# Kernel tuning notes

Hardware: AMD Instinct MI355X
Metric: run time of the kernel (lower is better)

Reference implementation:

```python
import jax, jax.numpy as jnp
import numpy as np

B, T, D = 4, 1024, 768
HW = 32            # H = W = sqrt(T)
DS = D // 16       # d_state = 48
CHUNK = 8          # items_each_chunk (must divide W)


def _ln(x, w, b, eps=1e-5):
    mu = x.mean(-1, keepdims=True)
    var = ((x - mu) ** 2).mean(-1, keepdims=True)
    return (x - mu) / jnp.sqrt(var + eps) * w + b


def _conv1x1(x, w):  # x: (B,C,H,W), w: (O,C)
    return jnp.einsum('bchw,oc->bohw', x, w)


def _dwconv(x, w, b, pad):  # depthwise conv, w: (C,1,k,k)
    y = jax.lax.conv_general_dilated(
        x, w, (1, 1), [(pad, pad), (pad, pad)],
        dimension_numbers=('NCHW', 'OIHW', 'NCHW'),
        feature_group_count=x.shape[1])
    if b is not None:
        y = y + b[None, :, None, None]
    return y


def _norm_gates(Gl, Gm, Gr):
    gl, gm, gr = jax.nn.sigmoid(Gl), jax.nn.sigmoid(Gm), jax.nn.sigmoid(Gr)
    s = gl + gm + gr
    s = s.at[:, :, 0, :].set(gm[:, :, 0, :] + gr[:, :, 0, :])    # top row: no h-1 neighbor
    s = s.at[:, :, -1, :].set(gl[:, :, -1, :] + gm[:, :, -1, :])  # bottom row: no h+1 neighbor
    s = jnp.maximum(s, 1e-7)
    return gl / s, gm / s, gr / s


def _gspn_scan(X, L, Gl, Gm, Gr, chunk):
    # GateRecurrent2dnoind: scan along W in independent chunks of `chunk` columns.
    # H[:, :, h, t] = L*X + Gl*Hprev[h-1] + Gm*Hprev[h] + Gr*Hprev[h+1], Hprev=0 at chunk start.
    b, c, h, w = X.shape
    nc = w // chunk

    def to_scan(a):  # (B,C,H,W) -> (chunk, B, C, H, nc)
        return a.reshape(b, c, h, nc, chunk).transpose(4, 0, 1, 2, 3)

    xs, ls, gls, gms, grs = map(to_scan, (X, L, Gl, Gm, Gr))

    def step(hprev, inp):
        x, l, gl, gm, gr = inp
        h_up = jnp.pad(hprev[:, :, :-1], ((0, 0), (0, 0), (1, 0), (0, 0)))
        h_dn = jnp.pad(hprev[:, :, 1:], ((0, 0), (0, 0), (0, 1), (0, 0)))
        hn = l * x + gl * h_up + gm * hprev + gr * h_dn
        return hn, hn

    _, ys = jax.lax.scan(step, jnp.zeros((b, c, h, nc), X.dtype), (xs, ls, gls, gms, grs))
    return ys.transpose(1, 2, 3, 4, 0).reshape(b, c, h, w)


def setup_inputs() -> dict:
    key = jax.random.key(0)
    ks = jax.random.split(key, 16)
    s = 0.02
    return {
        'hidden_states': jax.random.normal(ks[0], (B, T, D), jnp.float32),
        'norm_w': jnp.ones((D,), jnp.float32),
        'norm_b': jnp.zeros((D,), jnp.float32),
        'in_proj_w': jax.random.normal(ks[1], (D, D), jnp.float32) * s,
        'conv7_w': jax.random.normal(ks[2], (D, 1, 7, 7), jnp.float32) * s,
        'conv7_b': jnp.zeros((D,), jnp.float32),
        'xdown_w': jax.random.normal(ks[3], (DS, D), jnp.float32) * s,
        'wup_w': jax.random.normal(ks[4], (12 * D, DS), jnp.float32) * s,
        'lup_w': jax.random.normal(ks[5], (4 * D, DS), jnp.float32) * s,
        'uup_w': jax.random.normal(ks[6], (4 * D, DS), jnp.float32) * s,
        'dcoef_w': jax.random.normal(ks[7], (4 * D, DS), jnp.float32) * s,
        'm_w': jax.random.normal(ks[8], (4,), jnp.float32) * 0.25,
        'outconv_w': jax.random.normal(ks[9], (D, D), jnp.float32) * s,
        'outdconv_w': jax.random.normal(ks[10], (D, 1, 3, 3), jnp.float32) * s,
        'outproj_w': jax.random.normal(ks[11], (D, D), jnp.float32) * s,
    }


def reference(hidden_states, norm_w, norm_b, in_proj_w, conv7_w, conv7_b,
              xdown_w, wup_w, lup_w, uup_w, dcoef_w, m_w,
              outconv_w, outdconv_w, outproj_w):
    b, t, d = hidden_states.shape
    hh = ww = HW
    shortcut = hidden_states
    x = _ln(shortcut, norm_w, norm_b)                      # (B,T,D)
    x = x.transpose(0, 2, 1).reshape(b, d, hh, ww)         # (B,D,H,W)
    x = _conv1x1(x, in_proj_w)
    x = _dwconv(x, conv7_w, conv7_b, 3)
    xp = _conv1x1(x, xdown_w)                              # (B,ds,H,W)
    ws = _conv1x1(xp, wup_w)                               # (B,12D,H,W)
    Ls = _conv1x1(xp, lup_w)                               # (B,4D,H,W)
    Us = _conv1x1(xp, uup_w)
    Ds = _conv1x1(xp, dcoef_w)
    # 4 scan directions: [x, x^T, flip_w(x), flip_w(x^T)]
    x_hwwh = jnp.stack([x, x.transpose(0, 1, 3, 2)], axis=1)       # (B,2,D,H,W)
    xs = jnp.concatenate([x_hwwh, x_hwwh[..., ::-1]], axis=1)      # (B,4,D,H,W)
    xs = xs.reshape(b, 4 * d, hh, ww)
    Gl, Gm, Gr = ws[:, :4 * d], ws[:, 4 * d:8 * d], ws[:, 8 * d:]
    gl, gm, gr = _norm_gates(Gl, Gm, Gr)
    out = _gspn_scan(xs, Ls, gl, gm, gr, CHUNK)
    out = out * Us + xs * Ds
    out = out.reshape(b, 4, d, hh, ww)
    out = jnp.einsum('bkdhw,k->bdhw', out, m_w)            # m_conv (1x1 over 4 dirs)
    out = _conv1x1(out, outconv_w)
    out = _dwconv(out, outdconv_w, None, 1)
    out = out * jax.nn.relu(out)
    out = out.reshape(b, d, t).transpose(0, 2, 1)
    out = out @ outproj_w.T
    return out, shortcut
```

## Files before the change

### kernel.cpp

```cpp
#include <hip/hip_runtime.h>

typedef unsigned short u16;
typedef unsigned int u32;
typedef __attribute__((ext_vector_type(8))) short short8v;
typedef __attribute__((ext_vector_type(4))) float f32x4;

#define DD 768
#define PP 1024
#define NTOK 4096
#define ASN 520

__device__ __forceinline__ u16 f2bf(float f) {
  u32 u = __builtin_bit_cast(u32, f);
  u += 0x7fffu + ((u >> 16) & 1u);
  return (u16)(u >> 16);
}
__device__ __forceinline__ float b2f(u16 v) {
  return __builtin_bit_cast(float, (u32)v << 16);
}
__device__ __forceinline__ u32 pk_trunc(float fa, float fb) {
  return __builtin_amdgcn_perm(__builtin_bit_cast(u32, fa), __builtin_bit_cast(u32, fb), 0x07060302u);
}
__device__ __forceinline__ float ex8(const short8v& v, int j) {
  const u32 dw = ((const u32*)&v)[j >> 1];
  return __builtin_bit_cast(float, (j & 1) ? (dw & 0xffff0000u) : (dw << 16));
}

__global__ __launch_bounds__(256) void prep_ln_k(const float* __restrict__ hs,
                                                 const float* __restrict__ gw, const float* __restrict__ gb,
                                                 u16* __restrict__ lnout, float* __restrict__ shortcut,
                                                 const float* __restrict__ win, u16* __restrict__ wInB,
                                                 const float* __restrict__ wout, u16* __restrict__ wOutB,
                                                 const float* __restrict__ wprj, u16* __restrict__ wPrjB,
                                                 const float* __restrict__ xdw, u16* __restrict__ wXdB,
                                                 const float* __restrict__ wup, const float* __restrict__ lup,
                                                 const float* __restrict__ uup, const float* __restrict__ dco,
                                                 u16* __restrict__ wB) {
  const int id = blockIdx.x;
  const int t = threadIdx.x;
  if (id < 4096) {
    const int tok = id;
    const float* xr = hs + (size_t)tok * DD;
    float v0 = xr[t], v1 = xr[t + 256], v2 = xr[t + 512];
    float s = v0 + v1 + v2;
    float q = v0 * v0 + v1 * v1 + v2 * v2;
#pragma unroll
    for (int off = 32; off > 0; off >>= 1) {
      s += __shfl_down(s, off, 64);
      q += __shfl_down(q, off, 64);
    }
    __shared__ float ss[4], qs[4];
    const int wid = t >> 6, lane = t & 63;
    if (lane == 0) { ss[wid] = s; qs[wid] = q; }
    __syncthreads();
    const float st = ss[0] + ss[1] + ss[2] + ss[3];
    const float qt = qs[0] + qs[1] + qs[2] + qs[3];
    const float mu = st * (1.f / 768.f);
    const float var = qt * (1.f / 768.f) - mu * mu;
    const float rstd = rsqrtf(var + 1e-5f);
    float* sc = shortcut + (size_t)tok * DD;
    u16* lo = lnout + (size_t)tok * DD;
    sc[t] = v0; sc[t + 256] = v1; sc[t + 512] = v2;
    lo[t]       = f2bf((v0 - mu) * rstd * gw[t] + gb[t]);
    lo[t + 256] = f2bf((v1 - mu) * rstd * gw[t + 256] + gb[t + 256]);
    lo[t + 512] = f2bf((v2 - mu) * rstd * gw[t + 512] + gb[t + 512]);
    return;
  }
  const int id2 = id - 4096;
  if (id2 < 6912) {
    const int m = id2 / 2304;
    const int i = (id2 - m * 2304) * 256 + t;
    const float* s = (m == 0) ? win : (m == 1) ? wout : wprj;
    u16* d = (m == 0) ? wInB : (m == 1) ? wOutB : wPrjB;
    d[i] = f2bf(s[i]);
  } else if (id2 < 7104) {
    const int i = (id2 - 6912) * 256 + t;
    const int r = i / DD;
    wXdB[i] = (r < 48) ? f2bf(xdw[i]) : (u16)0;
  } else {
    const int c = id2 - 7104;
    u16* dst = wB + (size_t)c * 2048;
    for (int i = t; i < 2048; i += 256) {
      const int row = i >> 6, s = i & 63;
      u16 v = 0;
      if (row < 24 && s < 48) {
        const int k = row & 3, type = row >> 2;
        const int ch = k * DD + c;
        const float* src;
        if (type < 3) src = wup + ((size_t)(type * 3072 + ch)) * 48;
        else if (type == 3) src = lup + (size_t)ch * 48;
        else if (type == 4) src = uup + (size_t)ch * 48;
        else src = dco + (size_t)ch * 48;
        v = f2bf(src[s]);
      }
      dst[i] = v;
    }
  }
}

template <int BSRC>
__global__ __launch_bounds__(256) void gemm_bf16(const u16* __restrict__ A,
                                                 const u16* __restrict__ Bt,
                                                 void* __restrict__ outv, const int mode) {
  __shared__ u16 Al[64][40];
  __shared__ u16 BlF[144 * 40];
  const int t = threadIdx.x;
  const int ntile = blockIdx.x * 128;
  const int mtile = blockIdx.y * 64;
  const int bb = ntile >> 10, pq0 = ntile & 1023;
  const int wid = t >> 6, lane = t & 63;
  const int m0 = (wid & 1) * 32, n0 = (wid >> 1) * 64;
  const int l15 = lane & 15, quad = lane >> 4;
  f32x4 acc[2][4];
#pragma unroll
  for (int mi = 0; mi < 2; ++mi)
#pragma unroll
    for (int ni = 0; ni < 4; ++ni) acc[mi][ni] = (f32x4){0.f, 0.f, 0.f, 0.f};
  const int ra = t >> 2, sa = t & 3;
  const u16* ag = A + (size_t)(mtile + ra) * DD + sa * 8;
  const int rb = t >> 1, hb = t & 1;
  const u16* bg = Bt + (size_t)(ntile + rb) * DD + hb * 16;
  const int chp = t >> 4, tokg = t & 15, tok0 = tokg * 8;
  const u16* bgc = Bt + ((size_t)(bb * DD + chp * 2)) * PP + pq0 + tok0;
  for (int k0 = 0; k0 < DD; k0 += 32) {
    const uint4 av = *reinterpret_cast<const uint4*>(ag + k0);
    uint4 bv0, bv1;
    if (BSRC == 0) {
      bv0 = *reinterpret_cast<const uint4*>(bg + k0);
      bv1 = *reinterpret_cast<const uint4*>(bg + k0 + 8);
    } else {
      bv0 = *reinterpret_cast<const uint4*>(bgc + (size_t)k0 * PP);
      bv1 = *reinterpret_cast<const uint4*>(bgc + (size_t)(k0 + 1) * PP);
    }
    __syncthreads();
    *reinterpret_cast<uint4*>(&Al[ra][sa * 8]) = av;
    if (BSRC == 0) {
      const int pr = rb + (rb >> 3);
      *reinterpret_cast<uint4*>(&BlF[pr * 40 + hb * 16]) = bv0;
      *reinterpret_cast<uint4*>(&BlF[pr * 40 + hb * 16 + 8]) = bv1;
    } else {
      union { uint4 v; u16 u[8]; } ua, ub;
      ua.v = bv0; ub.v = bv1;
#pragma unroll
      for (int i2 = 0; i2 < 8; ++i2) {
        const int tk = tok0 + i2;
        *reinterpret_cast<u32*>(&BlF[(tk + (tk >> 3)) * 40 + chp * 2]) =
            (u32)ua.u[i2] | ((u32)ub.u[i2] << 16);
      }
    }
    __syncthreads();
    short8v af[2];
#pragma unroll
    for (int mi = 0; mi < 2; ++mi)
      af[mi] = *reinterpret_cast<const short8v*>(&Al[m0 + mi * 16 + l15][quad * 8]);
    short8v bfr[4];
#pragma unroll
    for (int ni = 0; ni < 4; ++ni) {
      const int tl = n0 + ni * 16 + l15;
      bfr[ni] = *reinterpret_cast<const short8v*>(&BlF[(tl + (tl >> 3)) * 40 + quad * 8]);
    }
#pragma unroll
    for (int mi = 0; mi < 2; ++mi)
#pragma unroll
      for (int ni = 0; ni < 4; ++ni)
        acc[mi][ni] = __builtin_amdgcn_mfma_f32_16x16x32_bf16(af[mi], bfr[ni], acc[mi][ni], 0, 0, 0);
  }
#pragma unroll
  for (int mi = 0; mi < 2; ++mi) {
#pragma unroll
    for (int ni = 0; ni < 4; ++ni) {
      const int ob = mtile + m0 + mi * 16 + quad * 4;
      const int pg = ntile + n0 + ni * 16 + l15;
      if (mode == 1) {
        *reinterpret_cast<f32x4*>((float*)outv + (size_t)pg * DD + ob) = acc[mi][ni];
      } else {
        const int pq = pg & 1023;
        u16* dstb = (u16*)outv;
#pragma unroll
        for (int r = 0; r < 4; ++r)
          dstb[((size_t)(bb * DD + ob + r)) * PP + pq] = f2bf(acc[mi][ni][r]);
      }
    }
  }
}

__global__ __launch_bounds__(256) void xdgemm_k(const u16* __restrict__ A,
                                                const u16* __restrict__ Ycm,
                                                u16* __restrict__ xpA) {
  __shared__ u16 Al[64][72];
  __shared__ u16 Bl[16][72];
  const int t = threadIdx.x;
  const int ntile = blockIdx.x * 16;
  const int bb = ntile >> 10, pq0 = ntile & 1023;
  const int wid = t >> 6, lane = t & 63, l15 = lane & 15, quad = lane >> 4;
  f32x4 acc = (f32x4){0.f, 0.f, 0.f, 0.f};
  const int arow = t >> 2, aks = (t & 3) * 16;
  const u16* ag = A + (size_t)arow * DD + aks;
  const int chp = t >> 3;
  const int tk0 = (t & 7) * 2;
  const u16* bg0 = Ycm + ((size_t)(bb * DD + chp * 2)) * PP + pq0 + tk0;
  for (int k0 = 0; k0 < DD; k0 += 64) {
    const uint4 a0 = *reinterpret_cast<const uint4*>(ag + k0);
    const uint4 a1 = *reinterpret_cast<const uint4*>(ag + k0 + 8);
    const u32 b0 = *reinterpret_cast<const u32*>(bg0 + (size_t)k0 * PP);
    const u32 b1 = *reinterpret_cast<const u32*>(bg0 + (size_t)(k0 + 1) * PP);
    __syncthreads();
    *reinterpret_cast<uint4*>(&Al[arow][aks]) = a0;
    *reinterpret_cast<uint4*>(&Al[arow][aks + 8]) = a1;
    *reinterpret_cast<u32*>(&Bl[tk0][chp * 2]) = (b0 & 0xffffu) | (b1 << 16);
    *reinterpret_cast<u32*>(&Bl[tk0 + 1][chp * 2]) = (b0 >> 16) | (b1 & 0xffff0000u);
    __syncthreads();
#pragma unroll
    for (int ks = 0; ks < 2; ++ks) {
      const short8v af = *reinterpret_cast<const short8v*>(&Al[wid * 16 + l15][ks * 32 + quad * 8]);
      const short8v bf = *reinterpret_cast<const short8v*>(&Bl[l15][ks * 32 + quad * 8]);
      acc = __builtin_amdgcn_mfma_f32_16x16x32_bf16(af, bf, acc, 0, 0, 0);
    }
  }
  const int pq = pq0 + l15;
  const int i = ((pq & 31) >> 4) * 512 + (pq >> 5) * 16 + (pq & 15);
  u16* dst = xpA + ((size_t)(bb * 1024 + i)) * 64 + wid * 16 + quad * 4;
  *reinterpret_cast<uint2*>(dst) = make_uint2(pk_trunc(acc[1], acc[0]), pk_trunc(acc[3], acc[2]));
}

__global__ __launch_bounds__(256) void dwconv7_k(const u16* __restrict__ x,
                                                 const float* __restrict__ wgt,
                                                 const float* __restrict__ bias,
                                                 u16* __restrict__ y) {
  const int bc = blockIdx.x;
  const int c = bc % DD;
  __shared__ float tile[38 * 38];
  __shared__ float wl[49];
  __shared__ float bsh[1];
  const int t = threadIdx.x;
  for (int i = t; i < 38 * 38; i += 256) tile[i] = 0.f;
  __syncthreads();
  const u16* xr = x + (size_t)bc * PP;
  for (int i = t; i < 512; i += 256) {
    const u32 v = reinterpret_cast<const u32*>(xr)[i];
    const int p0 = i * 2;
    const int h = p0 >> 5, w = p0 & 31;
    tile[(h + 3) * 38 + w + 3] = b2f((u16)v);
    tile[(h + 3) * 38 + w + 4] = b2f((u16)(v >> 16));
  }
  if (t < 49) wl[t] = wgt[c * 49 + t];
  if (t == 0) bsh[0] = bias[c];
  __syncthreads();
  u16* yo = y + (size_t)bc * PP;
  for (int i = t; i < 1024; i += 256) {
    const int h = i >> 5, w = i & 31;
    float acc = bsh[0];
#pragma unroll
    for (int kh = 0; kh < 7; ++kh)
#pragma unroll
      for (int kw = 0; kw < 7; ++kw)
        acc = fmaf(wl[kh * 7 + kw], tile[(h + kh) * 38 + (w + kw)], acc);
    yo[i] = f2bf(acc);
  }
}

__global__ __launch_bounds__(256) void dwconv3_k(const u16* __restrict__ x,
                                                 const float* __restrict__ wgt,
                                                 u16* __restrict__ y) {
  const int bc = blockIdx.x;
  const int c = bc % DD;
  __shared__ float tile[34 * 34];
  __shared__ float wl[9];
  const int t = threadIdx.x;
  for (int i = t; i < 34 * 34; i += 256) tile[i] = 0.f;
  __syncthreads();
  const u16* xr = x + (size_t)bc * PP;
  for (int i = t; i < 512; i += 256) {
    const u32 v = reinterpret_cast<const u32*>(xr)[i];
    const int p0 = i * 2;
    const int h = p0 >> 5, w = p0 & 31;
    tile[(h + 1) * 34 + w + 1] = b2f((u16)v);
    tile[(h + 1) * 34 + w + 2] = b2f((u16)(v >> 16));
  }
  if (t < 9) wl[t] = wgt[c * 9 + t];
  __syncthreads();
  u16* yo = y + (size_t)bc * PP;
  for (int i = t; i < 1024; i += 256) {
    const int h = i >> 5, w = i & 31;
    float acc = 0.f;
#pragma unroll
    for (int kh = 0; kh < 3; ++kh)
#pragma unroll
      for (int kw = 0; kw < 3; ++kw)
        acc = fmaf(wl[kh * 3 + kw], tile[(h + kh) * 34 + (w + kw)], acc);
    const float r = acc > 0.f ? acc * acc : 0.f;
    yo[i] = f2bf(r);
  }
}

__global__ __launch_bounds__(256, 5) void scan_k(const u16* __restrict__ y2b,
                                                 const u16* __restrict__ xpA,
                                                 const u16* __restrict__ wB,
                                                 const float* __restrict__ mwp,
                                                 u16* __restrict__ out1) {
  const int bid = blockIdx.x;
  const int bc = bid >> 1;
  const int half = bid & 1;
  const int b = bc / DD;
  const int c = bc - b * DD;
  __shared__ u16 act[24 * ASN];
  __shared__ u16 planeb[32][40];
  __shared__ u16 planeTb[32][40];
  __shared__ u16 outpb[2][16][34];
  const int t = threadIdx.x;
  const int wid = t >> 6, lane = t & 63, l15 = lane & 15, quad = lane >> 4;
  {
    const u16* yp = y2b + (size_t)bc * PP;
    for (int i = t; i < 512; i += 256) {
      const u32 v = reinterpret_cast<const u32*>(yp)[i];
      const int p0 = i * 2;
      const int hh = p0 >> 5, ww = p0 & 31;
      *reinterpret_cast<u32*>(&planeb[hh][ww]) = v;
      planeTb[ww][hh] = (u16)v;
      planeTb[ww + 1][hh] = (u16)(v >> 16);
    }
  }
  {
    const u16* wc = wB + (size_t)c * 2048;
    short8v bw[2][2];
#pragma unroll
    for (int nt = 0; nt < 2; ++nt)
#pragma unroll
      for (int ks = 0; ks < 2; ++ks)
        bw[nt][ks] = *reinterpret_cast<const short8v*>(wc + (nt * 16 + l15) * 64 + ks * 32 + quad * 8);
    const u16* ab = xpA + ((size_t)(b * 1024 + half * 512 + wid * 128)) * 64;
#pragma unroll 4
    for (int mt = 0; mt < 8; ++mt) {
      const u16* ar = ab + (mt * 16 + l15) * 64 + quad * 8;
      const short8v a0 = *reinterpret_cast<const short8v*>(ar);
      const short8v a1 = *reinterpret_cast<const short8v*>(ar + 32);
      f32x4 acc0 = {0.f, 0.f, 0.f, 0.f}, acc1 = {0.f, 0.f, 0.f, 0.f};
      acc0 = __builtin_amdgcn_mfma_f32_16x16x32_bf16(a0, bw[0][0], acc0, 0, 0, 0);
      acc0 = __builtin_amdgcn_mfma_f32_16x16x32_bf16(a1, bw[0][1], acc0, 0, 0, 0);
      acc1 = __builtin_amdgcn_mfma_f32_16x16x32_bf16(a0, bw[1][0], acc1, 0, 0, 0);
      acc1 = __builtin_amdgcn_mfma_f32_16x16x32_bf16(a1, bw[1][1], acc1, 0, 0, 0);
      const int qb = wid * 128 + mt * 16 + quad * 4;
      *reinterpret_cast<uint2*>(&act[l15 * ASN + qb]) =
          make_uint2(pk_trunc(acc0[1], acc0[0]), pk_trunc(acc0[3], acc0[2]));
      if (l15 < 8)
        *reinterpret_cast<uint2*>(&act[(16 + l15) * ASN + qb]) =
            make_uint2(pk_trunc(acc1[1], acc1[0]), pk_trunc(acc1[3], acc1[2]));
    }
  }
  __syncthreads();
  const int dpair = wid & 1;
  const int ncl = wid >> 1;
  const int d = lane >> 5;
  const int h = lane & 31;
  const int k = dpair * 2 + d;
  const float mw = mwp[k];
  const int base16 = h * 16 + ncl * 8;
  const short8v vGl = *reinterpret_cast<const short8v*>(&act[(0  + k) * ASN + base16]);
  const short8v vGm = *reinterpret_cast<const short8v*>(&act[(4  + k) * ASN + base16]);
  const short8v vGr = *reinterpret_cast<const short8v*>(&act[(8  + k) * ASN + base16]);
  const short8v vL  = *reinterpret_cast<const short8v*>(&act[(12 + k) * ASN + base16]);
  const short8v vU  = *reinterpret_cast<const short8v*>(&act[(16 + k) * ASN + base16]);
  const short8v vD  = *reinterpret_cast<const short8v*>(&act[(20 + k) * ASN + base16]);
  const int wst = dpair ? (24 - half * 16 - ncl * 8) : (half * 16 + ncl * 8);
  const u16* prowp = (d == 0) ? &planeb[h][wst] : &planeTb[h][wst];
  const short8v vP = *reinterpret_cast<const short8v*>(prowp);
  const bool top = (h == 0), bot = (h == 31);
  float gl[8], gm[8], gr[8], Lx[8], xvv[8];
#pragma unroll
  for (int j = 0; j < 8; ++j) {
    const float xv = ex8(vP, dpair ? (7 - j) : j);
    float el = __expf(-ex8(vGl, j));
    const float em = __expf(-ex8(vGm, j));
    float er = __expf(-ex8(vGr, j));
    if (top) el = 1e30f;
    if (bot) er = 1e30f;
    const float pl = 1.f + el, pm = 1.f + em, pr = 1.f + er;
    const float ul = pm * pr, um = pl * pr, ur = pl * pm;
    const float rcpS = __builtin_amdgcn_rcpf(ul + um + ur);
    gl[j] = ul * rcpS; gm[j] = um * rcpS; gr[j] = ur * rcpS;
    Lx[j] = ex8(vL, j) * xv;
    xvv[j] = xv;
  }
  float H = 0.f;
#pragma unroll
  for (int j = 0; j < 8; ++j) {
    const int Hb = __builtin_bit_cast(int, H);
    const float up = __builtin_bit_cast(float,
        __builtin_amdgcn_update_dpp(0, Hb, 0x138, 0xf, 0xf, true));
    const float dn = __builtin_bit_cast(float,
        __builtin_amdgcn_update_dpp(0, Hb, 0x130, 0xf, 0xf, true));
    H = fmaf(gl[j], up, fmaf(gm[j], H, fmaf(gr[j], dn, Lx[j])));
    float part = fmaf(H, ex8(vU, j), xvv[j] * ex8(vD, j)) * mw;
    part += __shfl_xor(part, 32, 64);
    if (d == 0)
      outpb[dpair][ncl * 8 + j][h] = (u16)(__builtin_bit_cast(u32, part) >> 16);
  }
  __syncthreads();
  const int hh = t >> 3, wp = t & 7;
  const float v0 = b2f(outpb[0][wp * 2][hh]) + b2f(outpb[1][wp * 2][hh]);
  const float v1 = b2f(outpb[0][wp * 2 + 1][hh]) + b2f(outpb[1][wp * 2 + 1][hh]);
  const u32 pk = pk_trunc(v1, v0);
  *reinterpret_cast<u32*>(out1 + (size_t)bc * PP + hh * 32 + half * 16 + wp * 2) = pk;
}

extern "C" void kernel_launch(void* const* d_in, const int* in_sizes, int n_in,
                              void* d_out, int out_size, void* d_ws, size_t ws_size,
                              hipStream_t stream) {
  const float* hs   = (const float*)d_in[0];
  const float* nw   = (const float*)d_in[1];
  const float* nb   = (const float*)d_in[2];
  const float* win  = (const float*)d_in[3];
  const float* c7w  = (const float*)d_in[4];
  const float* c7b  = (const float*)d_in[5];
  const float* xdw  = (const float*)d_in[6];
  const float* wupw = (const float*)d_in[7];
  const float* lupw = (const float*)d_in[8];
  const float* uupw = (const float*)d_in[9];
  const float* dcow = (const float*)d_in[10];
  const float* mww  = (const float*)d_in[11];
  const float* wout = (const float*)d_in[12];
  const float* odw  = (const float*)d_in[13];
  const float* wprj = (const float*)d_in[14];
  float* out0 = (float*)d_out;
  float* shortcut = out0 + (size_t)NTOK * DD;

  char* ws = (char*)d_ws;
  u16* lnA    = (u16*)(ws + 0);
  u16* wInB   = (u16*)(ws + 6291456);
  u16* wOutB  = (u16*)(ws + 7471104);
  u16* wPrjB  = (u16*)(ws + 8650752);
  u16* wB     = (u16*)(ws + 9830400);
  u16* wXdB   = (u16*)(ws + 12976128);
  u16* xpA    = (u16*)(ws + 13074432);
  u16* y1b    = (u16*)(ws + 13598720);
  u16* y2b    = (u16*)(ws + 19890176);
  u16* out1   = (u16*)(ws + 26181632);
  u16* y3b    = y1b;
  u16* y4b    = out1;

  prep_ln_k<<<11968, 256, 0, stream>>>(hs, nw, nb, lnA, shortcut,
                                       win, wInB, wout, wOutB, wprj, wPrjB,
                                       xdw, wXdB, wupw, lupw, uupw, dcow, wB);
  gemm_bf16<0><<<dim3(32, 12), 256, 0, stream>>>(wInB, lnA, y1b, 3);
  dwconv7_k<<<3072, 256, 0, stream>>>(y1b, c7w, c7b, y2b);
  xdgemm_k<<<256, 256, 0, stream>>>(wXdB, y2b, xpA);
  scan_k<<<6144, 256, 0, stream>>>(y2b, xpA, wB, mww, out1);
  gemm_bf16<1><<<dim3(32, 12), 256, 0, stream>>>(wOutB, out1, y3b, 3);
  dwconv3_k<<<3072, 256, 0, stream>>>(y3b, odw, y4b);
  gemm_bf16<1><<<dim3(32, 12), 256, 0, stream>>>(wPrjB, y4b, out0, 1);
}
```

Baseline: 249.1 us.

## Merge scan halves into one 512-thread block and register-block depthwise convs

The scan kernel now processes a full (batch, channel) plane per 512-thread block instead of two 256-thread half blocks. This stops the two halves from each reloading the plane and transposing it separately. It adds an XOR-swizzled shared activation buffer, reuses shared memory for the output staging, and uses permlane32_swap for the cross-half reduction when available. The 7x7 and 3x3 depthwise convs compute four output rows per thread so loaded tile rows are reused across vertically adjacent outputs. The larger scan block raises shared memory per block and adds an extra barrier, which may lower occupancy.

```diff
diff --git a/kernel.cpp b/kernel.cpp
--- a/kernel.cpp
+++ b/kernel.cpp
@@ -4,11 +4,11 @@
 typedef unsigned int u32;
 typedef __attribute__((ext_vector_type(8))) short short8v;
 typedef __attribute__((ext_vector_type(4))) float f32x4;
+typedef __attribute__((ext_vector_type(2))) unsigned u32x2v;
 
 #define DD 768
 #define PP 1024
 #define NTOK 4096
-#define ASN 520
 
 __device__ __forceinline__ u16 f2bf(float f) {
   u32 u = __builtin_bit_cast(u32, f);
@@ -247,16 +247,35 @@
   if (t == 0) bsh[0] = bias[c];
   __syncthreads();
   u16* yo = y + (size_t)bc * PP;
-  for (int i = t; i < 1024; i += 256) {
-    const int h = i >> 5, w = i & 31;
-    float acc = bsh[0];
-#pragma unroll
-    for (int kh = 0; kh < 7; ++kh)
-#pragma unroll
-      for (int kw = 0; kw < 7; ++kw)
-        acc = fmaf(wl[kh * 7 + kw], tile[(h + kh) * 38 + (w + kw)], acc);
-    yo[i] = f2bf(acc);
-  }
+  const int w = t & 31, hb = t >> 5;
+  const float bv = bsh[0];
+  float a0 = bv, a1 = bv, a2 = bv, a3 = bv;
+#pragma unroll
+  for (int rr = 0; rr < 10; ++rr) {
+    float row[7];
+#pragma unroll
+    for (int kw = 0; kw < 7; ++kw) row[kw] = tile[(hb * 4 + rr) * 38 + w + kw];
+    if (rr < 7) {
+#pragma unroll
+      for (int kw = 0; kw < 7; ++kw) a0 = fmaf(wl[rr * 7 + kw], row[kw], a0);
+    }
+    if (rr >= 1 && rr < 8) {
+#pragma unroll
+      for (int kw = 0; kw < 7; ++kw) a1 = fmaf(wl[(rr - 1) * 7 + kw], row[kw], a1);
+    }
+    if (rr >= 2 && rr < 9) {
+#pragma unroll
+      for (int kw = 0; kw < 7; ++kw) a2 = fmaf(wl[(rr - 2) * 7 + kw], row[kw], a2);
+    }
+    if (rr >= 3) {
+#pragma unroll
+      for (int kw = 0; kw < 7; ++kw) a3 = fmaf(wl[(rr - 3) * 7 + kw], row[kw], a3);
+    }
+  }
+  yo[(hb * 4 + 0) * 32 + w] = f2bf(a0);
+  yo[(hb * 4 + 1) * 32 + w] = f2bf(a1);
+  yo[(hb * 4 + 2) * 32 + w] = f2bf(a2);
+  yo[(hb * 4 + 3) * 32 + w] = f2bf(a3);
 }
 
 __global__ __launch_bounds__(256) void dwconv3_k(const u16* __restrict__ x,
@@ -280,45 +299,64 @@
   if (t < 9) wl[t] = wgt[c * 9 + t];
   __syncthreads();
   u16* yo = y + (size_t)bc * PP;
-  for (int i = t; i < 1024; i += 256) {
-    const int h = i >> 5, w = i & 31;
-    float acc = 0.f;
-#pragma unroll
-    for (int kh = 0; kh < 3; ++kh)
-#pragma unroll
-      for (int kw = 0; kw < 3; ++kw)
-        acc = fmaf(wl[kh * 3 + kw], tile[(h + kh) * 34 + (w + kw)], acc);
-    const float r = acc > 0.f ? acc * acc : 0.f;
-    yo[i] = f2bf(r);
-  }
-}
-
-__global__ __launch_bounds__(256, 5) void scan_k(const u16* __restrict__ y2b,
+  const int w = t & 31, hb = t >> 5;
+  float a0 = 0.f, a1 = 0.f, a2 = 0.f, a3 = 0.f;
+#pragma unroll
+  for (int rr = 0; rr < 6; ++rr) {
+    float row[3];
+#pragma unroll
+    for (int kw = 0; kw < 3; ++kw) row[kw] = tile[(hb * 4 + rr) * 34 + w + kw];
+    if (rr < 3) {
+#pragma unroll
+      for (int kw = 0; kw < 3; ++kw) a0 = fmaf(wl[rr * 3 + kw], row[kw], a0);
+    }
+    if (rr >= 1 && rr < 4) {
+#pragma unroll
+      for (int kw = 0; kw < 3; ++kw) a1 = fmaf(wl[(rr - 1) * 3 + kw], row[kw], a1);
+    }
+    if (rr >= 2 && rr < 5) {
+#pragma unroll
+      for (int kw = 0; kw < 3; ++kw) a2 = fmaf(wl[(rr - 2) * 3 + kw], row[kw], a2);
+    }
+    if (rr >= 3) {
+#pragma unroll
+      for (int kw = 0; kw < 3; ++kw) a3 = fmaf(wl[(rr - 3) * 3 + kw], row[kw], a3);
+    }
+  }
+  const float r0 = a0 > 0.f ? a0 * a0 : 0.f;
+  const float r1 = a1 > 0.f ? a1 * a1 : 0.f;
+  const float r2 = a2 > 0.f ? a2 * a2 : 0.f;
+  const float r3 = a3 > 0.f ? a3 * a3 : 0.f;
+  yo[(hb * 4 + 0) * 32 + w] = f2bf(r0);
+  yo[(hb * 4 + 1) * 32 + w] = f2bf(r1);
+  yo[(hb * 4 + 2) * 32 + w] = f2bf(r2);
+  yo[(hb * 4 + 3) * 32 + w] = f2bf(r3);
+}
+
+#define ACT_SWZ(row, col) ((col) ^ (((((col) >> 6) ^ (row)) & 7) << 3))
+__global__ __launch_bounds__(512, 6) void scan_k(const u16* __restrict__ y2b,
                                                  const u16* __restrict__ xpA,
                                                  const u16* __restrict__ wB,
                                                  const float* __restrict__ mwp,
                                                  u16* __restrict__ out1) {
-  const int bid = blockIdx.x;
-  const int bc = bid >> 1;
-  const int half = bid & 1;
+  const int bc = blockIdx.x;
   const int b = bc / DD;
   const int c = bc - b * DD;
-  __shared__ u16 act[24 * ASN];
-  __shared__ u16 planeb[32][40];
-  __shared__ u16 planeTb[32][40];
-  __shared__ u16 outpb[2][16][34];
+  __shared__ u16 act[24 * 1024];
+  __shared__ u16 pl[2560];
+  u16* planeb = pl;
+  u16* planeTb = pl + 1280;
+  u16* outpb = pl;
   const int t = threadIdx.x;
   const int wid = t >> 6, lane = t & 63, l15 = lane & 15, quad = lane >> 4;
   {
     const u16* yp = y2b + (size_t)bc * PP;
-    for (int i = t; i < 512; i += 256) {
-      const u32 v = reinterpret_cast<const u32*>(yp)[i];
-      const int p0 = i * 2;
-      const int hh = p0 >> 5, ww = p0 & 31;
-      *reinterpret_cast<u32*>(&planeb[hh][ww]) = v;
-      planeTb[ww][hh] = (u16)v;
-      planeTb[ww + 1][hh] = (u16)(v >> 16);
-    }
+    const u32 v = reinterpret_cast<const u32*>(yp)[t];
+    const int p0 = t * 2;
+    const int hh = p0 >> 5, ww = p0 & 31;
+    *reinterpret_cast<u32*>(&planeb[hh * 40 + ww]) = v;
+    planeTb[ww * 40 + hh] = (u16)v;
+    planeTb[(ww + 1) * 40 + hh] = (u16)(v >> 16);
   }
   {
     const u16* wc = wB + (size_t)c * 2048;
@@ -328,7 +366,7 @@
 #pragma unroll
       for (int ks = 0; ks < 2; ++ks)
         bw[nt][ks] = *reinterpret_cast<const short8v*>(wc + (nt * 16 + l15) * 64 + ks * 32 + quad * 8);
-    const u16* ab = xpA + ((size_t)(b * 1024 + half * 512 + wid * 128)) * 64;
+    const u16* ab = xpA + ((size_t)(b * 1024 + wid * 128)) * 64;
 #pragma unroll 4
     for (int mt = 0; mt < 8; ++mt) {
       const u16* ar = ab + (mt * 16 + l15) * 64 + quad * 8;
@@ -340,29 +378,32 @@
       acc1 = __builtin_amdgcn_mfma_f32_16x16x32_bf16(a0, bw[1][0], acc1, 0, 0, 0);
       acc1 = __builtin_amdgcn_mfma_f32_16x16x32_bf16(a1, bw[1][1], acc1, 0, 0, 0);
       const int qb = wid * 128 + mt * 16 + quad * 4;
-      *reinterpret_cast<uint2*>(&act[l15 * ASN + qb]) =
+      const int cs = ACT_SWZ(l15, qb);
+      *reinterpret_cast<uint2*>(&act[l15 * 1024 + cs]) =
           make_uint2(pk_trunc(acc0[1], acc0[0]), pk_trunc(acc0[3], acc0[2]));
       if (l15 < 8)
-        *reinterpret_cast<uint2*>(&act[(16 + l15) * ASN + qb]) =
+        *reinterpret_cast<uint2*>(&act[(16 + l15) * 1024 + cs]) =
             make_uint2(pk_trunc(acc1[1], acc1[0]), pk_trunc(acc1[3], acc1[2]));
     }
   }
   __syncthreads();
   const int dpair = wid & 1;
-  const int ncl = wid >> 1;
+  const int hc = wid >> 1;
   const int d = lane >> 5;
   const int h = lane & 31;
   const int k = dpair * 2 + d;
   const float mw = mwp[k];
-  const int base16 = h * 16 + ncl * 8;
-  const short8v vGl = *reinterpret_cast<const short8v*>(&act[(0  + k) * ASN + base16]);
-  const short8v vGm = *reinterpret_cast<const short8v*>(&act[(4  + k) * ASN + base16]);
-  const short8v vGr = *reinterpret_cast<const short8v*>(&act[(8  + k) * ASN + base16]);
-  const short8v vL  = *reinterpret_cast<const short8v*>(&act[(12 + k) * ASN + base16]);
-  const short8v vU  = *reinterpret_cast<const short8v*>(&act[(16 + k) * ASN + base16]);
-  const short8v vD  = *reinterpret_cast<const short8v*>(&act[(20 + k) * ASN + base16]);
-  const int wst = dpair ? (24 - half * 16 - ncl * 8) : (half * 16 + ncl * 8);
-  const u16* prowp = (d == 0) ? &planeb[h][wst] : &planeTb[h][wst];
+  const int colb = (hc >> 1) * 512 + h * 16 + (hc & 1) * 8;
+#define ACTP(row) (*reinterpret_cast<const short8v*>(&act[(row) * 1024 + ACT_SWZ((row), colb)]))
+  const short8v vGl = ACTP(0 + k);
+  const short8v vGm = ACTP(4 + k);
+  const short8v vGr = ACTP(8 + k);
+  const short8v vL  = ACTP(12 + k);
+  const short8v vU  = ACTP(16 + k);
+  const short8v vD  = ACTP(20 + k);
+#undef ACTP
+  const int wst = dpair ? (24 - hc * 8) : (hc * 8);
+  const u16* prowp = (d == 0) ? (planeb + h * 40 + wst) : (planeTb + h * 40 + wst);
   const short8v vP = *reinterpret_cast<const short8v*>(prowp);
   const bool top = (h == 0), bot = (h == 31);
   float gl[8], gm[8], gr[8], Lx[8], xvv[8];
@@ -374,13 +415,15 @@
     float er = __expf(-ex8(vGr, j));
     if (top) el = 1e30f;
     if (bot) er = 1e30f;
-    const float pl = 1.f + el, pm = 1.f + em, pr = 1.f + er;
-    const float ul = pm * pr, um = pl * pr, ur = pl * pm;
+    const float pl2 = 1.f + el, pm = 1.f + em, pr = 1.f + er;
+    const float ul = pm * pr, um = pl2 * pr, ur = pl2 * pm;
     const float rcpS = __builtin_amdgcn_rcpf(ul + um + ur);
     gl[j] = ul * rcpS; gm[j] = um * rcpS; gr[j] = ur * rcpS;
     Lx[j] = ex8(vL, j) * xv;
     xvv[j] = xv;
-  }
+    asm volatile("" : "+v"(gl[j]), "+v"(gm[j]), "+v"(gr[j]), "+v"(Lx[j]), "+v"(xvv[j]));
+  }
+  __syncthreads();
   float H = 0.f;
 #pragma unroll
   for (int j = 0; j < 8; ++j) {
@@ -391,16 +434,23 @@
         __builtin_amdgcn_update_dpp(0, Hb, 0x130, 0xf, 0xf, true));
     H = fmaf(gl[j], up, fmaf(gm[j], H, fmaf(gr[j], dn, Lx[j])));
     float part = fmaf(H, ex8(vU, j), xvv[j] * ex8(vD, j)) * mw;
+#if __has_builtin(__builtin_amdgcn_permlane32_swap)
+    {
+      u32x2v sw = __builtin_amdgcn_permlane32_swap(__builtin_bit_cast(u32, part),
+                                                   __builtin_bit_cast(u32, part), false, false);
+      part = __builtin_bit_cast(float, sw[0]) + __builtin_bit_cast(float, sw[1]);
+    }
+#else
     part += __shfl_xor(part, 32, 64);
+#endif
     if (d == 0)
-      outpb[dpair][ncl * 8 + j][h] = (u16)(__builtin_bit_cast(u32, part) >> 16);
-  }
-  __syncthreads();
-  const int hh = t >> 3, wp = t & 7;
-  const float v0 = b2f(outpb[0][wp * 2][hh]) + b2f(outpb[1][wp * 2][hh]);
-  const float v1 = b2f(outpb[0][wp * 2 + 1][hh]) + b2f(outpb[1][wp * 2 + 1][hh]);
-  const u32 pk = pk_trunc(v1, v0);
-  *reinterpret_cast<u32*>(out1 + (size_t)bc * PP + hh * 32 + half * 16 + wp * 2) = pk;
+      outpb[(dpair * 32 + hc * 8 + j) * 34 + h] = (u16)(__builtin_bit_cast(u32, part) >> 16);
+  }
+  __syncthreads();
+  const int hh2 = t >> 4, wp = t & 15;
+  const float v0 = b2f(outpb[(wp * 2) * 34 + hh2]) + b2f(outpb[(32 + wp * 2) * 34 + hh2]);
+  const float v1 = b2f(outpb[(wp * 2 + 1) * 34 + hh2]) + b2f(outpb[(32 + wp * 2 + 1) * 34 + hh2]);
+  *reinterpret_cast<u32*>(out1 + (size_t)bc * PP + hh2 * 32 + wp * 2) = pk_trunc(v1, v0);
 }
 
 extern "C" void kernel_launch(void* const* d_in, const int* in_sizes, int n_in,
@@ -444,7 +494,7 @@
   gemm_bf16<0><<<dim3(32, 12), 256, 0, stream>>>(wInB, lnA, y1b, 3);
   dwconv7_k<<<3072, 256, 0, stream>>>(y1b, c7w, c7b, y2b);
   xdgemm_k<<<256, 256, 0, stream>>>(wXdB, y2b, xpA);
-  scan_k<<<6144, 256, 0, stream>>>(y2b, xpA, wB, mww, out1);
+  scan_k<<<3072, 512, 0, stream>>>(y2b, xpA, wB, mww, out1);
   gemm_bf16<1><<<dim3(32, 12), 256, 0, stream>>>(wOutB, out1, y3b, 3);
   dwconv3_k<<<3072, 256, 0, stream>>>(y3b, odw, y4b);
   gemm_bf16<1><<<dim3(32, 12), 256, 0, stream>>>(wPrjB, y4b, out0, 1);
```

New measurement: 242.0 us. 2.9% less time.
